# Kernel optimization log

Hardware: AMD Instinct MI355X
Metric: run time of the kernel (lower is better)

The kernel has to match this reference:

```python
import math
import jax, jax.numpy as jnp
import numpy as np

DEGREE = 5
LN_EPS = 1e-5


def hermite_psi(C, r):
    # x_d = tanh(linspace(-1,1,C)) * (sqrt(2r+1)+1), shape [C]
    x_d = jnp.tanh(jnp.linspace(-1.0, 1.0, C)) * (math.sqrt(2 * r + 1) + 1.0)
    g = jnp.exp(-x_d ** 2 / 2.0)
    rows = [math.pi ** (-0.25) * g]
    if r > 0:
        rows.append(math.sqrt(2.0) * math.pi ** (-0.25) * x_d * g)
    for k in range(2, r + 1):
        rows.append(math.sqrt(2.0 / k) * x_d * rows[-1] - math.sqrt((k - 1) / k) * rows[-2])
    return jnp.stack(rows)  # [r+1, C]


def setup_inputs() -> dict:
    key = jax.random.key(0)
    k1, k2 = jax.random.split(key)
    B, C, H, W = 16, 512, 64, 64
    O = 512
    x = jax.random.normal(k1, (B, C, H, W), dtype=jnp.float32)
    ln_w = jnp.ones((C,), dtype=jnp.float32)
    ln_b = jnp.zeros((C,), dtype=jnp.float32)
    fc_w = jax.random.normal(k2, (O, C), dtype=jnp.float32) * (1.0 / math.sqrt(C))
    fc_b = jnp.zeros((O,), dtype=jnp.float32)
    return {"x": x, "ln_w": ln_w, "ln_b": ln_b, "fc_w": fc_w, "fc_b": fc_b}


def reference(x, ln_w, ln_b, fc_w, fc_b):
    B, C, H, W = x.shape
    O = fc_w.shape[0]
    # [B, HW, C]
    q = x.reshape(B, C, H * W).transpose(0, 2, 1)
    # LayerNorm over channels (biased variance, eps=1e-5)
    mu = q.mean(axis=-1, keepdims=True)
    var = ((q - mu) ** 2).mean(axis=-1, keepdims=True)
    q = (q - mu) / jnp.sqrt(var + LN_EPS) * ln_w + ln_b
    # Constant Hermite basis [r+1, C]
    psi = hermite_psi(C, DEGREE).astype(x.dtype)
    # Tiny cross-attention: scores [B, HW, r+1]
    scores = jnp.einsum('bnc,rc->bnr', q, psi) / math.sqrt(C)
    attn = jax.nn.softmax(scores, axis=-1)
    y = jnp.einsum('bnr,rc->bnc', attn, psi)  # [B, HW, C]
    # 1x1 conv == pointwise GEMM over channels
    out = jnp.einsum('bnc,oc->bon', y, fc_w) + fc_b[None, :, None]
    return out.reshape(B, O, H, W)
```

## Files before the change

kernel.cpp:

```cpp
#include <hip/hip_runtime.h>
#include <math.h>

#define C 512
#define NPIX 4096
#define BATCH 16
#define O 512
#define R 6
#define LN_EPS 1e-5f

typedef float vf4 __attribute__((ext_vector_type(4)));


__device__ __forceinline__ void hermite_rows(int c, float rows[R]) {
    float t = -1.0f + 2.0f * (float)c / 511.0f;
    float xd = tanhf(t) * 4.31662479035539984911f;
    float g = expf(-0.5f * xd * xd);
    const float pi_m14 = 0.75112554446494248286f;
    rows[0] = pi_m14 * g;
    rows[1] = 1.41421356237309504880f * pi_m14 * xd * g;
    #pragma unroll
    for (int k = 2; k <= 5; ++k)
        rows[k] = sqrtf(2.0f / k) * xd * rows[k - 1] - sqrtf((k - 1.0f) / k) * rows[k - 2];
}

__global__ __launch_bounds__(64) void setup_all(const float* __restrict__ lnw,
                                                const float* __restrict__ lnb,
                                                const float* __restrict__ fcw,
                                                const float* __restrict__ fcb,
                                                float* __restrict__ ws) {
    const int o = blockIdx.x;
    const int l = threadIdx.x;
    if (o < O) {
        float acc[R] = {0.f, 0.f, 0.f, 0.f, 0.f, 0.f};
        #pragma unroll
        for (int k = 0; k < 8; ++k) {
            int c = l + (k << 6);
            float rows[R];
            hermite_rows(c, rows);
            float w = fcw[o * C + c];
            #pragma unroll
            for (int r = 0; r < R; ++r) acc[r] += rows[r] * w;
        }
        #pragma unroll
        for (int r = 0; r < R; ++r)
            #pragma unroll
            for (int m = 32; m >= 1; m >>= 1) acc[r] += __shfl_xor(acc[r], m, 64);
        if (l == 0) {
            float bias = fcb[o];
            float* M = ws + 4112 + o * 8;
            #pragma unroll
            for (int r = 0; r < R; ++r) M[r] = acc[r] + bias;
        }
    } else {
        float sw[R] = {0.f, 0.f, 0.f, 0.f, 0.f, 0.f};
        float sb[R] = {0.f, 0.f, 0.f, 0.f, 0.f, 0.f};
        #pragma unroll
        for (int k = 0; k < 8; ++k) {
            int c = l + (k << 6);
            float rows[R];
            hermite_rows(c, rows);
            float w = lnw[c], bb = lnb[c];
            float* dst = ws + c * 8;
            #pragma unroll
            for (int r = 0; r < R; ++r) {
                float rw = rows[r] * w;
                dst[r] = rw;
                sw[r] += rw;
                sb[r] += rows[r] * bb;
            }
        }
        #pragma unroll
        for (int r = 0; r < R; ++r) {
            #pragma unroll
            for (int m = 32; m >= 1; m >>= 1) {
                sw[r] += __shfl_xor(sw[r], m, 64);
                sb[r] += __shfl_xor(sb[r], m, 64);
            }
        }
        if (l == 0) {
            #pragma unroll
            for (int r = 0; r < R; ++r) { ws[4096 + r] = sw[r]; ws[4104 + r] = sb[r]; }
        }
    }
}

__global__ __launch_bounds__(1024, 4) void fused_kernel(const float* __restrict__ x,
                                                        const float* __restrict__ ws,
                                                        float* __restrict__ out) {
    __shared__ float part[16][8][256];
    __shared__ float attn_s[R][256];
    const int tid = threadIdx.x;
    const int wv = tid >> 6;
    const int l = tid & 63;
    const int b = blockIdx.x >> 4;
    const int pxg = blockIdx.x & 15;
    const int n0 = pxg << 8;
    const int p4 = l << 2;
    const int wuni = __builtin_amdgcn_readfirstlane(wv);

    const float* xb = x + (((size_t)(b * C + (wuni << 5))) << 12) + n0 + p4;
    const float* wbase = ws + ((size_t)(wuni << 5) << 3);

    vf4 s = {0.f,0.f,0.f,0.f}, ss = s;
    vf4 a0 = s, a1 = s, a2 = s, a3 = s, a4 = s, a5 = s;
    #pragma unroll
    for (int i = 0; i < 32; ++i) {
        vf4 xv = *(const vf4*)(xb + ((size_t)i << 12));
        const float* wr = wbase + (i << 3);
        float w0 = wr[0], w1 = wr[1], w2 = wr[2];
        float w3 = wr[3], w4 = wr[4], w5 = wr[5];
        s  += xv;
        ss += xv * xv;
        a0 += xv * w0;
        a1 += xv * w1;
        a2 += xv * w2;
        a3 += xv * w3;
        a4 += xv * w4;
        a5 += xv * w5;
    }
    *(vf4*)&part[wv][0][p4] = s;
    *(vf4*)&part[wv][1][p4] = ss;
    *(vf4*)&part[wv][2][p4] = a0;
    *(vf4*)&part[wv][3][p4] = a1;
    *(vf4*)&part[wv][4][p4] = a2;
    *(vf4*)&part[wv][5][p4] = a3;
    *(vf4*)&part[wv][6][p4] = a4;
    *(vf4*)&part[wv][7][p4] = a5;
    __syncthreads();

    if (tid < 256) {
        float v[8];
        #pragma unroll
        for (int st = 0; st < 8; ++st) {
            float acc = 0.f;
            #pragma unroll
            for (int w = 0; w < 16; ++w) acc += part[w][st][tid];
            v[st] = acc;
        }
        float mu = v[0] * (1.0f / 512.0f);
        float var = v[1] * (1.0f / 512.0f) - mu * mu;
        float rsig = rsqrtf(var + LN_EPS);
        const float invsq = 0.04419417382415922f;
        float sc[R], mx = -1e30f;
        #pragma unroll
        for (int r = 0; r < R; ++r) {
            float swp = ws[4096 + r], sbp = ws[4104 + r];
            sc[r] = ((v[2 + r] - mu * swp) * rsig + sbp) * invsq;
            mx = fmaxf(mx, sc[r]);
        }
        float es = 0.f, at[R];
        #pragma unroll
        for (int r = 0; r < R; ++r) { at[r] = expf(sc[r] - mx); es += at[r]; }
        float inv = 1.0f / es;
        #pragma unroll
        for (int r = 0; r < R; ++r) attn_s[r][tid] = at[r] * inv;
    }
    __syncthreads();

    vf4 ar[R];
    #pragma unroll
    for (int r = 0; r < R; ++r) ar[r] = *(const vf4*)&attn_s[r][p4];

    const float* Ms = ws + 4112 + ((size_t)(wuni << 5) << 3);
    float* ob = out + (((size_t)(b * O + (wuni << 5))) << 12) + n0 + p4;
    #pragma unroll
    for (int j = 0; j < 32; ++j) {
        const float* mo = Ms + (j << 3);
        float m0 = mo[0], m1 = mo[1], m2 = mo[2];
        float m3 = mo[3], m4 = mo[4], m5 = mo[5];
        vf4 res = ar[0] * m0 + ar[1] * m1 + ar[2] * m2
                + ar[3] * m3 + ar[4] * m4 + ar[5] * m5;
        __builtin_nontemporal_store(res, (vf4*)(ob + ((size_t)j << 12)));
    }
}

extern "C" void kernel_launch(void* const* d_in, const int* in_sizes, int n_in,
                              void* d_out, int out_size, void* d_ws, size_t ws_size,
                              hipStream_t stream) {
    const float* x    = (const float*)d_in[0];
    const float* ln_w = (const float*)d_in[1];
    const float* ln_b = (const float*)d_in[2];
    const float* fc_w = (const float*)d_in[3];
    const float* fc_b = (const float*)d_in[4];
    float* out = (float*)d_out;
    float* ws = (float*)d_ws;

    setup_all<<<O + 1, 64, 0, stream>>>(ln_w, ln_b, fc_w, fc_b, ws);
    fused_kernel<<<BATCH * 16, 1024, 0, stream>>>(x, ws, out);
}
```

Before: 247.2 us.

## Split fused LN-attention-GEMM kernel into stats, softmax, and broadcast kernels

```diff
diff --git a/kernel.cpp b/kernel.cpp
--- a/kernel.cpp
+++ b/kernel.cpp
@@ -7,6 +7,7 @@
 #define O 512
 #define R 6
 #define LN_EPS 1e-5f
+#define ATTN_OFF 16384
 
 typedef float vf4 __attribute__((ext_vector_type(4)));
 
@@ -84,90 +85,108 @@
     }
 }
 
-__global__ __launch_bounds__(1024, 4) void fused_kernel(const float* __restrict__ x,
+__global__ __launch_bounds__(512, 2) void stats_partial(const float* __restrict__ x,
                                                         const float* __restrict__ ws,
-                                                        float* __restrict__ out) {
-    __shared__ float part[16][8][256];
-    __shared__ float attn_s[R][256];
-    const int tid = threadIdx.x;
-    const int wv = tid >> 6;
-    const int l = tid & 63;
+                                                        float* __restrict__ outp) {
+    const int t = threadIdx.x;
     const int b = blockIdx.x >> 4;
-    const int pxg = blockIdx.x & 15;
-    const int n0 = pxg << 8;
-    const int p4 = l << 2;
-    const int wuni = __builtin_amdgcn_readfirstlane(wv);
-
-    const float* xb = x + (((size_t)(b * C + (wuni << 5))) << 12) + n0 + p4;
-    const float* wbase = ws + ((size_t)(wuni << 5) << 3);
-
-    vf4 s = {0.f,0.f,0.f,0.f}, ss = s;
-    vf4 a0 = s, a1 = s, a2 = s, a3 = s, a4 = s, a5 = s;
-    #pragma unroll
-    for (int i = 0; i < 32; ++i) {
-        vf4 xv = *(const vf4*)(xb + ((size_t)i << 12));
-        const float* wr = wbase + (i << 3);
+    const int g = blockIdx.x & 15;
+    const int c0 = g << 5;
+    const float* xb = x + (((size_t)(b * C + c0)) << 12) + (t << 2);
+    const float* wb = ws + ((size_t)c0 << 3);
+
+    vf4 z = {0.f, 0.f, 0.f, 0.f};
+    vf4 a00=z,a01=z,a02=z,a03=z,a04=z,a05=z,a06=z,a07=z;
+    vf4 a10=z,a11=z,a12=z,a13=z,a14=z,a15=z,a16=z,a17=z;
+
+    #pragma unroll
+    for (int cc = 0; cc < 32; ++cc) {
+        const float* wr = wb + (cc << 3);
         float w0 = wr[0], w1 = wr[1], w2 = wr[2];
         float w3 = wr[3], w4 = wr[4], w5 = wr[5];
-        s  += xv;
-        ss += xv * xv;
-        a0 += xv * w0;
-        a1 += xv * w1;
-        a2 += xv * w2;
-        a3 += xv * w3;
-        a4 += xv * w4;
-        a5 += xv * w5;
-    }
-    *(vf4*)&part[wv][0][p4] = s;
-    *(vf4*)&part[wv][1][p4] = ss;
-    *(vf4*)&part[wv][2][p4] = a0;
-    *(vf4*)&part[wv][3][p4] = a1;
-    *(vf4*)&part[wv][4][p4] = a2;
-    *(vf4*)&part[wv][5][p4] = a3;
-    *(vf4*)&part[wv][6][p4] = a4;
-    *(vf4*)&part[wv][7][p4] = a5;
-    __syncthreads();
-
-    if (tid < 256) {
-        float v[8];
-        #pragma unroll
-        for (int st = 0; st < 8; ++st) {
-            float acc = 0.f;
-            #pragma unroll
-            for (int w = 0; w < 16; ++w) acc += part[w][st][tid];
-            v[st] = acc;
-        }
-        float mu = v[0] * (1.0f / 512.0f);
-        float var = v[1] * (1.0f / 512.0f) - mu * mu;
-        float rsig = rsqrtf(var + LN_EPS);
-        const float invsq = 0.04419417382415922f;
-        float sc[R], mx = -1e30f;
-        #pragma unroll
-        for (int r = 0; r < R; ++r) {
-            float swp = ws[4096 + r], sbp = ws[4104 + r];
-            sc[r] = ((v[2 + r] - mu * swp) * rsig + sbp) * invsq;
-            mx = fmaxf(mx, sc[r]);
-        }
-        float es = 0.f, at[R];
-        #pragma unroll
-        for (int r = 0; r < R; ++r) { at[r] = expf(sc[r] - mx); es += at[r]; }
-        float inv = 1.0f / es;
-        #pragma unroll
-        for (int r = 0; r < R; ++r) attn_s[r][tid] = at[r] * inv;
-    }
-    __syncthreads();
-
+        vf4 x0 = *(const vf4*)(xb + ((size_t)cc << 12));
+        vf4 x1 = *(const vf4*)(xb + ((size_t)cc << 12) + 2048);
+        a00 += x0;       a10 += x1;
+        a01 += x0 * x0;  a11 += x1 * x1;
+        a02 += x0 * w0;  a12 += x1 * w0;
+        a03 += x0 * w1;  a13 += x1 * w1;
+        a04 += x0 * w2;  a14 += x1 * w2;
+        a05 += x0 * w3;  a15 += x1 * w3;
+        a06 += x0 * w4;  a16 += x1 * w4;
+        a07 += x0 * w5;  a17 += x1 * w5;
+    }
+
+    float* pb = outp + (((size_t)(b * O + (g << 3))) << 12) + (t << 2);
+    *(vf4*)(pb + (0 << 12)) = a00;  *(vf4*)(pb + (0 << 12) + 2048) = a10;
+    *(vf4*)(pb + (1 << 12)) = a01;  *(vf4*)(pb + (1 << 12) + 2048) = a11;
+    *(vf4*)(pb + (2 << 12)) = a02;  *(vf4*)(pb + (2 << 12) + 2048) = a12;
+    *(vf4*)(pb + (3 << 12)) = a03;  *(vf4*)(pb + (3 << 12) + 2048) = a13;
+    *(vf4*)(pb + (4 << 12)) = a04;  *(vf4*)(pb + (4 << 12) + 2048) = a14;
+    *(vf4*)(pb + (5 << 12)) = a05;  *(vf4*)(pb + (5 << 12) + 2048) = a15;
+    *(vf4*)(pb + (6 << 12)) = a06;  *(vf4*)(pb + (6 << 12) + 2048) = a16;
+    *(vf4*)(pb + (7 << 12)) = a07;  *(vf4*)(pb + (7 << 12) + 2048) = a17;
+}
+
+__global__ __launch_bounds__(256) void combine_softmax(const float* __restrict__ outp,
+                                                       const float* __restrict__ ws,
+                                                       float* __restrict__ attn) {
+    const int tid = threadIdx.x;
+    const int b = blockIdx.x >> 4;
+    const int n = ((blockIdx.x & 15) << 8) + tid;
+    const float* pb = outp + (((size_t)(b * O)) << 12) + n;
+
+    float v[8] = {0.f, 0.f, 0.f, 0.f, 0.f, 0.f, 0.f, 0.f};
+    #pragma unroll
+    for (int g = 0; g < 16; ++g)
+        #pragma unroll
+        for (int st = 0; st < 8; ++st)
+            v[st] += pb[(size_t)((g << 3) + st) << 12];
+
+    float mu = v[0] * (1.0f / 512.0f);
+    float var = v[1] * (1.0f / 512.0f) - mu * mu;
+    float rsig = rsqrtf(var + LN_EPS);
+    const float invsq = 0.04419417382415922f;
+    float sc[R], mx = -1e30f;
+    #pragma unroll
+    for (int r = 0; r < R; ++r) {
+        float swp = ws[4096 + r], sbp = ws[4104 + r];
+        sc[r] = ((v[2 + r] - mu * swp) * rsig + sbp) * invsq;
+        mx = fmaxf(mx, sc[r]);
+    }
+    float es = 0.f, at[R];
+    #pragma unroll
+    for (int r = 0; r < R; ++r) { at[r] = expf(sc[r] - mx); es += at[r]; }
+    float inv = 1.0f / es;
+    #pragma unroll
+    for (int r = 0; r < R; ++r)
+        attn[(((size_t)(b * 6 + r)) << 12) + n] = at[r] * inv;
+}
+
+__global__ __launch_bounds__(256) void bcast_kernel(const float* __restrict__ ws,
+                                                    float* __restrict__ out) {
+    const int tid = threadIdx.x;
+    const int bid = blockIdx.x;
+    const int b = bid >> 8;
+    const int pxg = (bid >> 6) & 3;
+    const int og = bid & 63;
+    const int n = (pxg << 10) + (tid << 2);
+
+    const float* attn = ws + ATTN_OFF;
     vf4 ar[R];
     #pragma unroll
-    for (int r = 0; r < R; ++r) ar[r] = *(const vf4*)&attn_s[r][p4];
-
-    const float* Ms = ws + 4112 + ((size_t)(wuni << 5) << 3);
-    float* ob = out + (((size_t)(b * O + (wuni << 5))) << 12) + n0 + p4;
-    #pragma unroll
-    for (int j = 0; j < 32; ++j) {
-        const float* mo = Ms + (j << 3);
-        float m0 = mo[0], m1 = mo[1], m2 = mo[2];
-        float m3 = mo[3], m4 = mo[4], m5 = mo[5];
+    for (int r = 0; r < R; ++r)
+        ar[r] = *(const vf4*)(attn + (((size_t)(b * 6 + r)) << 12) + n);
+
+    float* ob = out + (((size_t)(b * O + (og << 3))) << 12) + n;
+    #pragma unroll
+    for (int j = 0; j < 8; ++j) {
+        int o = (og << 3) + j;
+        float m0 = ws[4112 + o * 8 + 0];
+        float m1 = ws[4112 + o * 8 + 1];
+        float m2 = ws[4112 + o * 8 + 2];
+        float m3 = ws[4112 + o * 8 + 3];
+        float m4 = ws[4112 + o * 8 + 4];
+        float m5 = ws[4112 + o * 8 + 5];
         vf4 res = ar[0] * m0 + ar[1] * m1 + ar[2] * m2
                 + ar[3] * m3 + ar[4] * m4 + ar[5] * m5;
         __builtin_nontemporal_store(res, (vf4*)(ob + ((size_t)j << 12)));
@@ -186,5 +205,7 @@
     float* ws = (float*)d_ws;
 
     setup_all<<<O + 1, 64, 0, stream>>>(ln_w, ln_b, fc_w, fc_b, ws);
-    fused_kernel<<<BATCH * 16, 1024, 0, stream>>>(x, ws, out);
-}
+    stats_partial<<<BATCH * 16, 512, 0, stream>>>(x, ws, out);
+    combine_softmax<<<BATCH * 16, 256, 0, stream>>>(out, ws, ws + ATTN_OFF);
+    bcast_kernel<<<4096, 256, 0, stream>>>(ws, out);
+}
```

New measurement: 280.8 us. 13.6% more time.
